# Optimization experiments

Hardware: AMD Instinct MI355X
Metric: run time of the kernel (lower is better)

The kernel has to match this reference:

```python
import jax, jax.numpy as jnp
import numpy as np

N_NODES = 50000  # 4 node types x 12500
N_PER = 12500
E = 600000
H = 128
IN_DIMS = [128, 128, 64, 64]


def setup_inputs() -> dict:
    key = jax.random.key(0)
    ks = jax.random.split(key, 16)
    inp = {}
    for i, d in enumerate(IN_DIMS):
        inp[f"feat{i}"] = jax.random.normal(ks[i], (N_PER, d), dtype=jnp.float32)
        # xavier_normal-ish init, gain 1.414
        std = 1.414 * np.sqrt(2.0 / (d + H))
        inp[f"W_fc{i}"] = jax.random.normal(ks[4 + i], (d, H), dtype=jnp.float32) * std
        inp[f"b_fc{i}"] = jnp.zeros((H,), dtype=jnp.float32)
    inp["src"] = jax.random.randint(ks[8], (E,), 0, N_NODES, dtype=jnp.int32)
    inp["dst"] = jax.random.randint(ks[9], (E,), 0, N_NODES, dtype=jnp.int32)
    inp["e_feat"] = jax.random.randint(ks[10], (E,), 0, 36, dtype=jnp.int32)
    inp["b_g0"] = jnp.zeros((H,), dtype=jnp.float32)  # GraphConv layer0 (weight=False, bias)
    inp["W_g1"] = jax.random.normal(ks[11], (H, H), dtype=jnp.float32) * np.sqrt(1.0 / H)
    inp["b_g1"] = jnp.zeros((H,), dtype=jnp.float32)
    return inp


def _degree_norms(src, dst):
    ones = jnp.ones((src.shape[0],), dtype=jnp.float32)
    deg_out = jax.ops.segment_sum(ones, src, num_segments=N_NODES)
    deg_in = jax.ops.segment_sum(ones, dst, num_segments=N_NODES)
    # DGL norm='both': D_out^{-1/2} on src side, D_in^{-1/2} on dst side (clamp 0-degree)
    out_norm = jax.lax.rsqrt(jnp.maximum(deg_out, 1.0))
    in_norm = jax.lax.rsqrt(jnp.maximum(deg_in, 1.0))
    return out_norm, in_norm


def _gcn_aggregate(h, src, dst, out_norm, in_norm):
    m = (h * out_norm[:, None])[src]                      # [E, H] gather
    agg = jax.ops.segment_sum(m, dst, num_segments=N_NODES)
    return agg * in_norm[:, None]


def reference(feat0, feat1, feat2, feat3,
              W_fc0, b_fc0, W_fc1, b_fc1, W_fc2, b_fc2, W_fc3, b_fc3,
              src, dst, e_feat, b_g0, W_g1, b_g1):
    # per-node-type linear projections, then concat along node dim
    h = jnp.concatenate([
        feat0 @ W_fc0 + b_fc0,
        feat1 @ W_fc1 + b_fc1,
        feat2 @ W_fc2 + b_fc2,
        feat3 @ W_fc3 + b_fc3,
    ], axis=0)  # [N_NODES, H]

    out_norm, in_norm = _degree_norms(src, dst)
    # GraphConv layer 0: weight=False, bias, activation (dropout p=0 -> identity)
    h = jax.nn.relu(_gcn_aggregate(h, src, dst, out_norm, in_norm) + b_g0)
    # GraphConv layer 1: aggregate, then linear weight + bias, activation
    h = jax.nn.relu(_gcn_aggregate(h, src, dst, out_norm, in_norm) @ W_g1 + b_g1)

    e = e_feat.astype(jnp.float32)  # e_feat.reshape(-1,1).float() in original
    # forward graph: msg = ft + sum_{r in 0..4} where(e==r, ft, 0) = ft * (1 + 1{e in 0..4})
    w_fwd = 1.0 + sum((e == float(r)).astype(jnp.float32) for r in (0, 1, 2, 3, 4))
    agg_a = jax.ops.segment_sum(h[src] * w_fwd[:, None], dst, num_segments=N_NODES)
    # transpose graph (reversed edges, same e): msg = sum_{r in {6,14,30}} where(e==r, ft, 0)
    w_bwd = sum((e == float(r)).astype(jnp.float32) for r in (6, 14, 30))
    agg_b = jax.ops.segment_sum(h[dst] * w_bwd[:, None], src, num_segments=N_NODES)
    return agg_a + agg_b
```

## Files before the change

### kernel.cpp

```cpp
#include <hip/hip_runtime.h>
#include <hip/hip_bf16.h>

#define N_NODES 50000
#define N_PER   12500
#define E_EDGES 600000
#define HDIM    128

#define NBLK_FC    ((N_PER + 63) / 64)
#define NBLK_G     ((N_NODES + 63) / 64)
#define NBLK_NODE  ((N_NODES + 255) / 256)
#define MASK31  0x7fffffff

#define HQD 64
#define HSL_D (E_EDGES / HQD)
#define NBLK_DB (HQD * 4)

typedef __attribute__((ext_vector_type(8))) short bfrag;
typedef __attribute__((ext_vector_type(4))) float ffrag;

__device__ __forceinline__ unsigned short f2bf(float f) {
    union { float f; unsigned u; } x; x.f = f;
    unsigned r = x.u + 0x7fffu + ((x.u >> 16) & 1u);
    return (unsigned short)(r >> 16);
}
__device__ __forceinline__ float lo_bf(unsigned v) { return __uint_as_float(v << 16); }
__device__ __forceinline__ float hi_bf(unsigned v) { return __uint_as_float(v & 0xffff0000u); }
__device__ __forceinline__ unsigned pack2(float a, float b) {
    return (unsigned)f2bf(a) | ((unsigned)f2bf(b) << 16);
}
__device__ __forceinline__ float onrm_of(int deg) {
    return rsqrtf(fmaxf((float)deg, 1.0f));
}

__device__ __forceinline__ void acc8_add(float* acc, uint4 v) {
    acc[0] += lo_bf(v.x); acc[1] += hi_bf(v.x);
    acc[2] += lo_bf(v.y); acc[3] += hi_bf(v.y);
    acc[4] += lo_bf(v.z); acc[5] += hi_bf(v.z);
    acc[6] += lo_bf(v.w); acc[7] += hi_bf(v.w);
}
__device__ __forceinline__ void acc8_addw(float* acc, uint4 v, float w) {
    acc[0] += lo_bf(v.x) * w; acc[1] += hi_bf(v.x) * w;
    acc[2] += lo_bf(v.y) * w; acc[3] += hi_bf(v.y) * w;
    acc[4] += lo_bf(v.z) * w; acc[5] += hi_bf(v.z) * w;
    acc[6] += lo_bf(v.w) * w; acc[7] += hi_bf(v.w) * w;
}

__global__ __launch_bounds__(256) void prep_kernel(
    const float* __restrict__ W0, const float* __restrict__ W1,
    const float* __restrict__ W2, const float* __restrict__ W3,
    const float* __restrict__ Wg,
    const int* __restrict__ src, const int* __restrict__ dst,
    const int* __restrict__ ef,
    unsigned short* __restrict__ Wp,
    unsigned short* __restrict__ partialS,
    unsigned short* __restrict__ partialD,
    unsigned char*  __restrict__ partialB) {
    __shared__ unsigned hist[N_PER];
    int b = blockIdx.x;
    if (b < NBLK_DB) {
        const int q = b >> 2;
        const int p = b & 3;
        const int g0 = p * N_PER;
        for (int j = threadIdx.x; j < N_PER; j += 256) hist[j] = 0;
        __syncthreads();
        const int e0 = q * HSL_D;
        for (int i = e0 + threadIdx.x; i < e0 + HSL_D; i += 256) {
            int d = dst[i], t = ef[i], s = src[i];
            unsigned rd = (unsigned)(d - g0);
            if (rd < (unsigned)N_PER) atomicAdd(&hist[rd], 1u);
            unsigned rs = (unsigned)(s - g0);
            if (rs < (unsigned)N_PER) {
                unsigned inc = 0x10000u
                             + ((t == 6 || t == 14 || t == 30) ? 0x400u : 0u);
                atomicAdd(&hist[rs], inc);
            }
        }
        __syncthreads();
        for (int j = threadIdx.x; j < N_PER; j += 256) {
            unsigned h = hist[j];
            partialD[(size_t)q * N_NODES + g0 + j] = (unsigned short)(h & 0x3FFu);
            partialB[(size_t)q * N_NODES + g0 + j] = (unsigned char)((h >> 10) & 0x3Fu);
            partialS[(size_t)q * N_NODES + g0 + j] = (unsigned short)(h >> 16);
        }
    } else {
        int tid = (b - NBLK_DB) * 256 + threadIdx.x;
        const float* W; int D, base, off;
        if      (tid < 2048) { W = W0; D = 128; base = 0;    off = 0;     }
        else if (tid < 4096) { W = W1; D = 128; base = 2048; off = 16384; }
        else if (tid < 5120) { W = W2; D = 64;  base = 4096; off = 32768; }
        else if (tid < 6144) { W = W3; D = 64;  base = 5120; off = 40960; }
        else                 { W = Wg; D = 128; base = 6144; off = 49152; }
        int t2 = tid - base;
        int KT = D / 32;
        int l = t2 & 63;
        int tt = t2 >> 6;
        int kt = tt % KT, n0 = tt / KT;
        int n = n0 * 16 + (l & 15);
        int kb = kt * 32 + (l >> 4) * 8;
#pragma unroll
        for (int j = 0; j < 8; ++j)
            Wp[(size_t)off + (size_t)t2 * 8 + j] = f2bf(W[(size_t)(kb + j) * 128 + n]);
    }
}

__global__ __launch_bounds__(256) void plane_prefix_kernel(
    unsigned short* __restrict__ partialD, unsigned char* __restrict__ partialB,
    const unsigned short* __restrict__ partialS,
    int* __restrict__ degD, int* __restrict__ degB,
    int* __restrict__ scanD, int* __restrict__ scanB,
    int* __restrict__ blocksumD, int* __restrict__ blocksumB,
    float* __restrict__ onrm_buf) {
    const int t = threadIdx.x;
    const int n = blockIdx.x * 256 + t;
    int dD = 0, dB = 0;
    if (n < N_NODES) {
        int run = 0;
#pragma unroll
        for (int q = 0; q < HQD; ++q) {
            size_t ix = (size_t)q * N_NODES + n;
            int c = partialD[ix];
            partialD[ix] = (unsigned short)run;
            run += c;
        }
        dD = run; degD[n] = run;
        run = 0;
#pragma unroll
        for (int q = 0; q < HQD; ++q) {
            size_t ix = (size_t)q * N_NODES + n;
            int c = partialB[ix];
            partialB[ix] = (unsigned char)run;
            run += c;
        }
        dB = run; degB[n] = run;
        int dS = 0;
#pragma unroll
        for (int q = 0; q < HQD; ++q)
            dS += partialS[(size_t)q * N_NODES + n];
        onrm_buf[n] = onrm_of(dS);
    }
    __shared__ int sD[256], sB[256];
    sD[t] = dD; sB[t] = dB;
    __syncthreads();
    for (int off = 1; off < 256; off <<= 1) {
        int xD = (t >= off) ? sD[t - off] : 0;
        int xB = (t >= off) ? sB[t - off] : 0;
        __syncthreads();
        sD[t] += xD; sB[t] += xB;
        __syncthreads();
    }
    if (n < N_NODES) {
        scanD[n] = sD[t] - dD;
        scanB[n] = sB[t] - dB;
    }
    if (t == 255) {
        blocksumD[blockIdx.x] = sD[255];
        blocksumB[blockIdx.x] = sB[255];
    }
}

__global__ __launch_bounds__(256) void base_add_kernel(
    const int* __restrict__ blocksumD, const int* __restrict__ blocksumB,
    int* __restrict__ scanD, int* __restrict__ scanB) {
    __shared__ int sD[256], sB[256];
    const int t = threadIdx.x;
    const int bid = blockIdx.x;
    sD[t] = (t < bid) ? blocksumD[t] : 0;
    sB[t] = (t < bid) ? blocksumB[t] : 0;
    __syncthreads();
    for (int off = 128; off >= 1; off >>= 1) {
        if (t < off) { sD[t] += sD[t + off]; sB[t] += sB[t + off]; }
        __syncthreads();
    }
    const int n = bid * 256 + t;
    if (n < N_NODES) { scanD[n] += sD[0]; scanB[n] += sB[0]; }
}

template<int D>
__device__ __forceinline__ void fc_body(
    int blk, int tid,
    const float* __restrict__ X,
    const unsigned short* __restrict__ Wp,
    const float* __restrict__ bias,
    const float* __restrict__ onrm,
    unsigned short* __restrict__ outbf,
    int rows)
{
    constexpr int KT = D / 32;
    const int lane = tid & 63;
    const int wave = tid >> 6;
    const int m = lane & 15, q = lane >> 4;
    const int rbase = blk * 64 + wave * 16;
    const int row = rbase + m;

    bfrag afr[KT];
#pragma unroll
    for (int kt = 0; kt < KT; ++kt) {
        bfrag a;
        if (row < rows) {
            const float* xp = X + (size_t)row * D + kt * 32 + q * 8;
            float4 u0 = *(const float4*)xp;
            float4 u1 = *(const float4*)(xp + 4);
            a[0] = (short)f2bf(u0.x); a[1] = (short)f2bf(u0.y);
            a[2] = (short)f2bf(u0.z); a[3] = (short)f2bf(u0.w);
            a[4] = (short)f2bf(u1.x); a[5] = (short)f2bf(u1.y);
            a[6] = (short)f2bf(u1.z); a[7] = (short)f2bf(u1.w);
        } else {
#pragma unroll
            for (int t = 0; t < 8; ++t) a[t] = 0;
        }
        afr[kt] = a;
    }

    ffrag acc[8];
#pragma unroll
    for (int n0 = 0; n0 < 8; ++n0)
#pragma unroll
        for (int t = 0; t < 4; ++t) acc[n0][t] = 0.f;

#pragma unroll
    for (int n0 = 0; n0 < 8; ++n0)
#pragma unroll
        for (int kt = 0; kt < KT; ++kt) {
            bfrag bfr = *(const bfrag*)(Wp + ((size_t)(n0 * KT + kt) * 64 + lane) * 8);
            acc[n0] = __builtin_amdgcn_mfma_f32_16x16x32_bf16(afr[kt], bfr, acc[n0], 0, 0, 0);
        }

#pragma unroll
    for (int n0 = 0; n0 < 8; ++n0) {
        const int col = n0 * 16 + m;
        const float bj = bias[col];
#pragma unroll
        for (int r = 0; r < 4; ++r) {
            int orow = rbase + q * 4 + r;
            if (orow < rows)
                outbf[(size_t)orow * 128 + col] =
                    f2bf((acc[n0][r] + bj) * onrm[orow]);
        }
    }
}

__global__ __launch_bounds__(1024) void scatfc_kernel(
    const int* __restrict__ src, const int* __restrict__ dst,
    const int* __restrict__ ef,
    const unsigned short* __restrict__ prefD,
    const unsigned char*  __restrict__ prefB,
    const int* __restrict__ scanD, const int* __restrict__ scanB,
    int* __restrict__ bucket, int* __restrict__ bucketB,
    const float* __restrict__ f0, const float* __restrict__ f1,
    const float* __restrict__ f2, const float* __restrict__ f3,
    const unsigned short* __restrict__ Wp,
    const float* __restrict__ b0, const float* __restrict__ b1,
    const float* __restrict__ b2, const float* __restrict__ b3,
    const float* __restrict__ onrm_buf,
    unsigned short* __restrict__ Abf)
{
    __shared__ unsigned offP[N_PER];
    const int b = blockIdx.x;
    if (b < NBLK_DB) {
        const int q = b >> 2;
        const int p = b & 3;
        const int g0 = p * N_PER;
        for (int j = threadIdx.x; j < N_PER; j += 1024)
            offP[j] = (unsigned)(scanD[g0 + j] + (int)prefD[(size_t)q * N_NODES + g0 + j])
                    | ((unsigned)prefB[(size_t)q * N_NODES + g0 + j] << 20);
        __syncthreads();
        const int e0 = q * HSL_D;
        for (int i = e0 + threadIdx.x; i < e0 + HSL_D; i += 1024) {
            int s = src[i], d = dst[i], t = ef[i];
            unsigned rd = (unsigned)(d - g0);
            if (rd < (unsigned)N_PER) {
                unsigned old = atomicAdd(&offP[rd], 1u);
                bucket[old & 0xFFFFFu] = s | ((t <= 4) ? 0x80000000 : 0);
            }
            if (t == 6 || t == 14 || t == 30) {
                unsigned rs = (unsigned)(s - g0);
                if (rs < (unsigned)N_PER) {
                    unsigned old = atomicAdd(&offP[rs], 1u << 20);
                    bucketB[scanB[s] + (int)(old >> 20)] = d;
                }
            }
        }
    } else {
        int ft = (b - NBLK_DB) * 4 + (threadIdx.x >> 8);
        int tid = threadIdx.x & 255;
        int which = ft / NBLK_FC;
        int blk = ft - which * NBLK_FC;
        if (which == 0)
            fc_body<128>(blk, tid, f0, Wp,         b0, onrm_buf,
                         Abf + (size_t)0 * N_PER * HDIM, N_PER);
        else if (which == 1)
            fc_body<128>(blk, tid, f1, Wp + 16384, b1, onrm_buf + N_PER,
                         Abf + (size_t)1 * N_PER * HDIM, N_PER);
        else if (which == 2)
            fc_body<64>(blk, tid, f2, Wp + 32768, b2, onrm_buf + 2 * N_PER,
                        Abf + (size_t)2 * N_PER * HDIM, N_PER);
        else
            fc_body<64>(blk, tid, f3, Wp + 40960, b3, onrm_buf + 3 * N_PER,
                        Abf + (size_t)3 * N_PER * HDIM, N_PER);
    }
}

__global__ __launch_bounds__(256) void agg0_kernel(
    const uint4* __restrict__ A,
    const int* __restrict__ bucket, const int* __restrict__ scanD,
    const int* __restrict__ degD,
    const float* __restrict__ onrm_buf, const float* __restrict__ b_g0,
    uint4* __restrict__ B) {
    int idx = blockIdx.x * blockDim.x + threadIdx.x;
    int n = idx >> 4, j8 = idx & 15;
    const int cnt = degD[n];
    const int* bk = bucket + scanD[n];
    float acc[8] = {0.f, 0.f, 0.f, 0.f, 0.f, 0.f, 0.f, 0.f};
    int i = 0;
    for (; i + 8 <= cnt; i += 8) {
        uint4 v[8];
#pragma unroll
        for (int k = 0; k < 8; ++k)
            v[k] = A[(size_t)(bk[i + k] & MASK31) * 16 + j8];
#pragma unroll
        for (int k = 0; k < 8; ++k) acc8_add(acc, v[k]);
    }
    if (i + 4 <= cnt) {
        uint4 v[4];
#pragma unroll
        for (int k = 0; k < 4; ++k)
            v[k] = A[(size_t)(bk[i + k] & MASK31) * 16 + j8];
#pragma unroll
        for (int k = 0; k < 4; ++k) acc8_add(acc, v[k]);
        i += 4;
    }
    for (; i < cnt; ++i)
        acc8_add(acc, A[(size_t)(bk[i] & MASK31) * 16 + j8]);
    float inr = onrm_of(cnt);
    float onr = onrm_buf[n];
    const float* bg = b_g0 + j8 * 8;
    float r[8];
#pragma unroll
    for (int k = 0; k < 8; ++k)
        r[k] = fmaxf(acc[k] * inr + bg[k], 0.f) * onr;
    uint4 o;
    o.x = pack2(r[0], r[1]); o.y = pack2(r[2], r[3]);
    o.z = pack2(r[4], r[5]); o.w = pack2(r[6], r[7]);
    B[(size_t)n * 16 + j8] = o;
}

__global__ __launch_bounds__(256) void gemmg_kernel(
    const unsigned short* __restrict__ Bbf,
    const unsigned short* __restrict__ Wp,
    unsigned short* __restrict__ BWbf)
{
    const int lane = threadIdx.x & 63;
    const int wave = threadIdx.x >> 6;
    const int m = lane & 15, q = lane >> 4;
    const int rbase = blockIdx.x * 64 + wave * 16;
    const int row = rbase + m;

    bfrag afr[4];
#pragma unroll
    for (int kt = 0; kt < 4; ++kt) {
        if (row < N_NODES)
            afr[kt] = *(const bfrag*)(Bbf + (size_t)row * 128 + kt * 32 + q * 8);
        else {
#pragma unroll
            for (int t = 0; t < 8; ++t) afr[kt][t] = 0;
        }
    }

    ffrag acc[8];
#pragma unroll
    for (int n0 = 0; n0 < 8; ++n0)
#pragma unroll
        for (int t = 0; t < 4; ++t) acc[n0][t] = 0.f;

#pragma unroll
    for (int n0 = 0; n0 < 8; ++n0)
#pragma unroll
        for (int kt = 0; kt < 4; ++kt) {
            bfrag bfr = *(const bfrag*)(Wp + ((size_t)(n0 * 4 + kt) * 64 + lane) * 8);
            acc[n0] = __builtin_amdgcn_mfma_f32_16x16x32_bf16(afr[kt], bfr, acc[n0], 0, 0, 0);
        }

#pragma unroll
    for (int n0 = 0; n0 < 8; ++n0) {
        const int col = n0 * 16 + m;
#pragma unroll
        for (int r = 0; r < 4; ++r) {
            int orow = rbase + q * 4 + r;
            if (orow < N_NODES)
                BWbf[(size_t)orow * 128 + col] = f2bf(acc[n0][r]);
        }
    }
}

__global__ __launch_bounds__(256) void agg1_kernel(
    const uint4* __restrict__ BW,
    const int* __restrict__ bucket, const int* __restrict__ scanD,
    const int* __restrict__ degD,
    const float* __restrict__ b_g1,
    uint4* __restrict__ H) {
    int idx = blockIdx.x * blockDim.x + threadIdx.x;
    int n = idx >> 4, j8 = idx & 15;
    const int cnt = degD[n];
    const int* bk = bucket + scanD[n];
    float acc[8] = {0.f, 0.f, 0.f, 0.f, 0.f, 0.f, 0.f, 0.f};
    int i = 0;
    for (; i + 8 <= cnt; i += 8) {
        uint4 v[8];
#pragma unroll
        for (int k = 0; k < 8; ++k)
            v[k] = BW[(size_t)(bk[i + k] & MASK31) * 16 + j8];
#pragma unroll
        for (int k = 0; k < 8; ++k) acc8_add(acc, v[k]);
    }
    if (i + 4 <= cnt) {
        uint4 v[4];
#pragma unroll
        for (int k = 0; k < 4; ++k)
            v[k] = BW[(size_t)(bk[i + k] & MASK31) * 16 + j8];
#pragma unroll
        for (int k = 0; k < 4; ++k) acc8_add(acc, v[k]);
        i += 4;
    }
    for (; i < cnt; ++i)
        acc8_add(acc, BW[(size_t)(bk[i] & MASK31) * 16 + j8]);
    float inr = onrm_of(cnt);
    const float* bg = b_g1 + j8 * 8;
    float r[8];
#pragma unroll
    for (int k = 0; k < 8; ++k)
        r[k] = fmaxf(acc[k] * inr + bg[k], 0.f);
    uint4 o;
    o.x = pack2(r[0], r[1]); o.y = pack2(r[2], r[3]);
    o.z = pack2(r[4], r[5]); o.w = pack2(r[6], r[7]);
    H[(size_t)n * 16 + j8] = o;
}

__global__ __launch_bounds__(256) void final_kernel(
    const uint4* __restrict__ H,
    const int* __restrict__ bucket, const int* __restrict__ scanD,
    const int* __restrict__ degD,
    const int* __restrict__ bucketB, const int* __restrict__ scanB,
    const int* __restrict__ degB,
    float4* __restrict__ out4) {
    int idx = blockIdx.x * blockDim.x + threadIdx.x;
    int n = idx >> 4, j8 = idx & 15;
    float acc[8] = {0.f, 0.f, 0.f, 0.f, 0.f, 0.f, 0.f, 0.f};
    const int cnt = degD[n];
    const int* bk = bucket + scanD[n];
    int i = 0;
    for (; i + 8 <= cnt; i += 8) {
        int c[8]; uint4 v[8];
#pragma unroll
        for (int k = 0; k < 8; ++k) c[k] = bk[i + k];
#pragma unroll
        for (int k = 0; k < 8; ++k)
            v[k] = H[(size_t)(c[k] & MASK31) * 16 + j8];
#pragma unroll
        for (int k = 0; k < 8; ++k)
            acc8_addw(acc, v[k], (c[k] < 0) ? 2.0f : 1.0f);
    }
    if (i + 4 <= cnt) {
        int c[4]; uint4 v[4];
#pragma unroll
        for (int k = 0; k < 4; ++k) c[k] = bk[i + k];
#pragma unroll
        for (int k = 0; k < 4; ++k)
            v[k] = H[(size_t)(c[k] & MASK31) * 16 + j8];
#pragma unroll
        for (int k = 0; k < 4; ++k)
            acc8_addw(acc, v[k], (c[k] < 0) ? 2.0f : 1.0f);
        i += 4;
    }
    for (; i < cnt; ++i) {
        int c = bk[i];
        acc8_addw(acc, H[(size_t)(c & MASK31) * 16 + j8], (c < 0) ? 2.0f : 1.0f);
    }
    const int cb = degB[n];
    const int* bkB = bucketB + scanB[n];
    for (int k = 0; k < cb; ++k) {
        int d = bkB[k];
        acc8_add(acc, H[(size_t)d * 16 + j8]);
    }
    float4 o0 = {acc[0], acc[1], acc[2], acc[3]};
    float4 o1 = {acc[4], acc[5], acc[6], acc[7]};
    out4[(size_t)n * 32 + j8 * 2]     = o0;
    out4[(size_t)n * 32 + j8 * 2 + 1] = o1;
}

extern "C" void kernel_launch(void* const* d_in, const int* in_sizes, int n_in,
                              void* d_out, int out_size, void* d_ws, size_t ws_size,
                              hipStream_t stream) {
    const float* feat[4]  = {(const float*)d_in[0], (const float*)d_in[3],
                             (const float*)d_in[6], (const float*)d_in[9]};
    const float* W_fc[4]  = {(const float*)d_in[1], (const float*)d_in[4],
                             (const float*)d_in[7], (const float*)d_in[10]};
    const float* b_fc[4]  = {(const float*)d_in[2], (const float*)d_in[5],
                             (const float*)d_in[8], (const float*)d_in[11]};
    const int*   src      = (const int*)d_in[12];
    const int*   dst      = (const int*)d_in[13];
    const int*   efeat    = (const int*)d_in[14];
    const float* b_g0     = (const float*)d_in[15];
    const float* W_g1     = (const float*)d_in[16];
    const float* b_g1     = (const float*)d_in[17];
    float* out = (float*)d_out;

    char* p = (char*)d_ws;
    unsigned short* Abf = (unsigned short*)p; p += (size_t)N_NODES * HDIM * 2;
    unsigned short* Bbf = (unsigned short*)p; p += (size_t)N_NODES * HDIM * 2;
    unsigned short* Wp  = (unsigned short*)p; p += (size_t)65536 * 2;
    int* bucket  = (int*)p; p += (size_t)E_EDGES * 4;
    int* bucketB = (int*)p; p += (size_t)E_EDGES * 4;
    unsigned short* partialS = (unsigned short*)p; p += (size_t)HQD * N_NODES * 2;
    unsigned short* partialD = (unsigned short*)p; p += (size_t)HQD * N_NODES * 2;
    unsigned char*  partialB = (unsigned char*)p;  p += (size_t)HQD * N_NODES;
    int* degD  = (int*)p; p += (size_t)N_NODES * 4;
    int* degB  = (int*)p; p += (size_t)N_NODES * 4;
    int* scanD = (int*)p; p += (size_t)N_NODES * 4;
    int* scanB = (int*)p; p += (size_t)N_NODES * 4;
    float* onrm_buf = (float*)p; p += (size_t)N_NODES * 4;
    int* blocksumD = (int*)p; p += 256 * 4;
    int* blocksumB = (int*)p; p += 256 * 4;

    const unsigned short* Wpg = Wp + 49152;

    prep_kernel<<<NBLK_DB + 32, 256, 0, stream>>>(
        W_fc[0], W_fc[1], W_fc[2], W_fc[3], W_g1, src, dst, efeat,
        Wp, partialS, partialD, partialB);

    plane_prefix_kernel<<<NBLK_NODE, 256, 0, stream>>>(
        partialD, partialB, partialS, degD, degB, scanD, scanB,
        blocksumD, blocksumB, onrm_buf);

    base_add_kernel<<<NBLK_NODE, 256, 0, stream>>>(
        blocksumD, blocksumB, scanD, scanB);

    scatfc_kernel<<<NBLK_DB + NBLK_FC, 1024, 0, stream>>>(
        src, dst, efeat, partialD, partialB, scanD, scanB, bucket, bucketB,
        feat[0], feat[1], feat[2], feat[3], Wp,
        b_fc[0], b_fc[1], b_fc[2], b_fc[3], onrm_buf, Abf);

    const int grid_node = (N_NODES * 16) / 256;

    agg0_kernel<<<grid_node, 256, 0, stream>>>(
        (const uint4*)Abf, bucket, scanD, degD, onrm_buf, b_g0, (uint4*)Bbf);

    gemmg_kernel<<<NBLK_G, 256, 0, stream>>>(Bbf, Wpg, Abf);

    agg1_kernel<<<grid_node, 256, 0, stream>>>(
        (const uint4*)Abf, bucket, scanD, degD, b_g1, (uint4*)Bbf);

    final_kernel<<<grid_node, 256, 0, stream>>>(
        (const uint4*)Bbf, bucket, scanD, degD, bucketB, scanB, degB, (float4*)out);
}
```

Measured before the change: 253.0 us.

## Fuse layer-1 weight GEMM into layer-0 aggregation kernel via shared-memory tile

The layer-0 aggregation kernel now stages each block's 16 aggregated node rows in shared memory and runs the 128x128 bf16 MFMA projection right there. This removes the separate GEMM launch and its round trip of the intermediate through global memory. The aggregate/GEMM buffers are swapped to match. Separately, the prep kernel moves to 1024-thread blocks with fewer weight-packing blocks.

```diff
diff --git a/kernel.cpp b/kernel.cpp
--- a/kernel.cpp
+++ b/kernel.cpp
@@ -7,7 +7,6 @@
 #define HDIM    128
 
 #define NBLK_FC    ((N_PER + 63) / 64)
-#define NBLK_G     ((N_NODES + 63) / 64)
 #define NBLK_NODE  ((N_NODES + 255) / 256)
 #define MASK31  0x7fffffff
 
@@ -45,7 +44,7 @@
     acc[6] += lo_bf(v.w) * w; acc[7] += hi_bf(v.w) * w;
 }
 
-__global__ __launch_bounds__(256) void prep_kernel(
+__global__ __launch_bounds__(1024) void prep_kernel(
     const float* __restrict__ W0, const float* __restrict__ W1,
     const float* __restrict__ W2, const float* __restrict__ W3,
     const float* __restrict__ Wg,
@@ -61,10 +60,10 @@
         const int q = b >> 2;
         const int p = b & 3;
         const int g0 = p * N_PER;
-        for (int j = threadIdx.x; j < N_PER; j += 256) hist[j] = 0;
+        for (int j = threadIdx.x; j < N_PER; j += 1024) hist[j] = 0;
         __syncthreads();
         const int e0 = q * HSL_D;
-        for (int i = e0 + threadIdx.x; i < e0 + HSL_D; i += 256) {
+        for (int i = e0 + threadIdx.x; i < e0 + HSL_D; i += 1024) {
             int d = dst[i], t = ef[i], s = src[i];
             unsigned rd = (unsigned)(d - g0);
             if (rd < (unsigned)N_PER) atomicAdd(&hist[rd], 1u);
@@ -76,14 +75,14 @@
             }
         }
         __syncthreads();
-        for (int j = threadIdx.x; j < N_PER; j += 256) {
+        for (int j = threadIdx.x; j < N_PER; j += 1024) {
             unsigned h = hist[j];
             partialD[(size_t)q * N_NODES + g0 + j] = (unsigned short)(h & 0x3FFu);
             partialB[(size_t)q * N_NODES + g0 + j] = (unsigned char)((h >> 10) & 0x3Fu);
             partialS[(size_t)q * N_NODES + g0 + j] = (unsigned short)(h >> 16);
         }
     } else {
-        int tid = (b - NBLK_DB) * 256 + threadIdx.x;
+        int tid = (b - NBLK_DB) * 1024 + threadIdx.x;
         const float* W; int D, base, off;
         if      (tid < 2048) { W = W0; D = 128; base = 0;    off = 0;     }
         else if (tid < 4096) { W = W1; D = 128; base = 2048; off = 16384; }
@@ -300,14 +299,18 @@
     }
 }
 
-__global__ __launch_bounds__(256) void agg0_kernel(
+__global__ __launch_bounds__(256) void agg0g_kernel(
     const uint4* __restrict__ A,
     const int* __restrict__ bucket, const int* __restrict__ scanD,
     const int* __restrict__ degD,
     const float* __restrict__ onrm_buf, const float* __restrict__ b_g0,
-    uint4* __restrict__ B) {
-    int idx = blockIdx.x * blockDim.x + threadIdx.x;
-    int n = idx >> 4, j8 = idx & 15;
+    const unsigned short* __restrict__ Wp,
+    unsigned short* __restrict__ BW) {
+    __shared__ uint4 Bt[256];
+    const int tdx = threadIdx.x;
+    const int nloc = tdx >> 4, j8 = tdx & 15;
+    const int n = blockIdx.x * 16 + nloc;
+
     const int cnt = degD[n];
     const int* bk = bucket + scanD[n];
     float acc[8] = {0.f, 0.f, 0.f, 0.f, 0.f, 0.f, 0.f, 0.f};
@@ -331,6 +334,7 @@
     }
     for (; i < cnt; ++i)
         acc8_add(acc, A[(size_t)(bk[i] & MASK31) * 16 + j8]);
+
     float inr = onrm_of(cnt);
     float onr = onrm_buf[n];
     const float* bg = b_g0 + j8 * 8;
@@ -341,53 +345,39 @@
     uint4 o;
     o.x = pack2(r[0], r[1]); o.y = pack2(r[2], r[3]);
     o.z = pack2(r[4], r[5]); o.w = pack2(r[6], r[7]);
-    B[(size_t)n * 16 + j8] = o;
-}
-
-__global__ __launch_bounds__(256) void gemmg_kernel(
-    const unsigned short* __restrict__ Bbf,
-    const unsigned short* __restrict__ Wp,
-    unsigned short* __restrict__ BWbf)
-{
-    const int lane = threadIdx.x & 63;
-    const int wave = threadIdx.x >> 6;
+    Bt[j8 * 16 + nloc] = o;
+    __syncthreads();
+
+    const int lane = tdx & 63;
+    const int wave = tdx >> 6;
     const int m = lane & 15, q = lane >> 4;
-    const int rbase = blockIdx.x * 64 + wave * 16;
-    const int row = rbase + m;
 
     bfrag afr[4];
 #pragma unroll
-    for (int kt = 0; kt < 4; ++kt) {
-        if (row < N_NODES)
-            afr[kt] = *(const bfrag*)(Bbf + (size_t)row * 128 + kt * 32 + q * 8);
-        else {
-#pragma unroll
-            for (int t = 0; t < 8; ++t) afr[kt][t] = 0;
-        }
-    }
-
-    ffrag acc[8];
-#pragma unroll
-    for (int n0 = 0; n0 < 8; ++n0)
-#pragma unroll
-        for (int t = 0; t < 4; ++t) acc[n0][t] = 0.f;
-
-#pragma unroll
-    for (int n0 = 0; n0 < 8; ++n0)
+    for (int kt = 0; kt < 4; ++kt)
+        afr[kt] = *(const bfrag*)(Bt + (kt * 4 + q) * 16 + m);
+
+    ffrag acc2[2];
+#pragma unroll
+    for (int t2 = 0; t2 < 2; ++t2) {
+#pragma unroll
+        for (int t = 0; t < 4; ++t) acc2[t2][t] = 0.f;
+        const int n0 = wave * 2 + t2;
 #pragma unroll
         for (int kt = 0; kt < 4; ++kt) {
             bfrag bfr = *(const bfrag*)(Wp + ((size_t)(n0 * 4 + kt) * 64 + lane) * 8);
-            acc[n0] = __builtin_amdgcn_mfma_f32_16x16x32_bf16(afr[kt], bfr, acc[n0], 0, 0, 0);
-        }
-
-#pragma unroll
-    for (int n0 = 0; n0 < 8; ++n0) {
-        const int col = n0 * 16 + m;
-#pragma unroll
-        for (int r = 0; r < 4; ++r) {
-            int orow = rbase + q * 4 + r;
-            if (orow < N_NODES)
-                BWbf[(size_t)orow * 128 + col] = f2bf(acc[n0][r]);
+            acc2[t2] = __builtin_amdgcn_mfma_f32_16x16x32_bf16(afr[kt], bfr, acc2[t2], 0, 0, 0);
+        }
+    }
+
+    const int rowbase = blockIdx.x * 16;
+#pragma unroll
+    for (int t2 = 0; t2 < 2; ++t2) {
+        const int col = (wave * 2 + t2) * 16 + m;
+#pragma unroll
+        for (int rr = 0; rr < 4; ++rr) {
+            const int row = rowbase + q * 4 + rr;
+            BW[(size_t)row * 128 + col] = f2bf(acc2[t2][rr]);
         }
     }
 }
@@ -523,7 +513,7 @@
 
     const unsigned short* Wpg = Wp + 49152;
 
-    prep_kernel<<<NBLK_DB + 32, 256, 0, stream>>>(
+    prep_kernel<<<NBLK_DB + 8, 1024, 0, stream>>>(
         W_fc[0], W_fc[1], W_fc[2], W_fc[3], W_g1, src, dst, efeat,
         Wp, partialS, partialD, partialB);
 
@@ -541,14 +531,13 @@
 
     const int grid_node = (N_NODES * 16) / 256;
 
-    agg0_kernel<<<grid_node, 256, 0, stream>>>(
-        (const uint4*)Abf, bucket, scanD, degD, onrm_buf, b_g0, (uint4*)Bbf);
-
-    gemmg_kernel<<<NBLK_G, 256, 0, stream>>>(Bbf, Wpg, Abf);
+    agg0g_kernel<<<grid_node, 256, 0, stream>>>(
+        (const uint4*)Abf, bucket, scanD, degD, onrm_buf, b_g0, Wpg,
+        Bbf);
 
     agg1_kernel<<<grid_node, 256, 0, stream>>>(
-        (const uint4*)Abf, bucket, scanD, degD, b_g1, (uint4*)Bbf);
+        (const uint4*)Bbf, bucket, scanD, degD, b_g1, (uint4*)Abf);
 
     final_kernel<<<grid_node, 256, 0, stream>>>(
-        (const uint4*)Bbf, bucket, scanD, degD, bucketB, scanB, degB, (float4*)out);
-}
+        (const uint4*)Abf, bucket, scanD, degD, bucketB, scanB, degB, (float4*)out);
+}
```

After: 233.6 us. -7.6%, faster.
